# Optimization experiments

Hardware: AMD Instinct MI355X
Metric: run time of the kernel (lower is better)

## Reference

```python
import jax, jax.numpy as jnp
import numpy as np

B, S, HID = 2, 1024, 2048
N_HEADS, N_KV, HEAD_DIM = 32, 4, 128
BLOCK, MAX_BLOCKS = 32, 128
EPS = 1e-6
ROPE_THETA = 1e6


def _rmsnorm(x, w):
    # per-head RMSNorm over head_dim (Qwen3MoeRMSNorm)
    var = jnp.mean(x * x, axis=-1, keepdims=True)
    return x * jax.lax.rsqrt(var + EPS) * w


def _rotate_half(x):
    h = x.shape[-1] // 2
    return jnp.concatenate([-x[..., h:], x[..., :h]], axis=-1)


def setup_inputs() -> dict:
    key = jax.random.key(0)
    ks = jax.random.split(key, 8)
    hidden_states = jax.random.normal(ks[0], (B, S, HID), dtype=jnp.float32)
    wq = jax.random.normal(ks[1], (N_HEADS * HEAD_DIM, HID), dtype=jnp.float32) * 0.02
    wk = jax.random.normal(ks[2], (N_KV * HEAD_DIM, HID), dtype=jnp.float32) * 0.02
    wv = jax.random.normal(ks[3], (N_KV * HEAD_DIM, HID), dtype=jnp.float32) * 0.02
    wo = jax.random.normal(ks[4], (HID, N_HEADS * HEAD_DIM), dtype=jnp.float32) * 0.02
    q_norm_w = 1.0 + 0.01 * jax.random.normal(ks[5], (HEAD_DIM,), dtype=jnp.float32)
    k_norm_w = 1.0 + 0.01 * jax.random.normal(ks[6], (HEAD_DIM,), dtype=jnp.float32)
    # RoPE tables (rotate-half / llama convention)
    inv_freq = 1.0 / (ROPE_THETA ** (jnp.arange(0, HEAD_DIM, 2, dtype=jnp.float32) / HEAD_DIM))
    t = jnp.arange(S, dtype=jnp.float32)
    freqs = jnp.outer(t, inv_freq)  # [S, HEAD_DIM/2]
    emb = jnp.concatenate([freqs, freqs], axis=-1)  # [S, HEAD_DIM]
    cos, sin = jnp.cos(emb), jnp.sin(emb)
    # page table: B sequences x (S/BLOCK) blocks, distinct block ids
    page_table = jnp.arange(B * (S // BLOCK), dtype=jnp.int32).reshape(B, S // BLOCK)
    return {"hidden_states": hidden_states, "wq": wq, "wk": wk, "wv": wv, "wo": wo,
            "q_norm_w": q_norm_w, "k_norm_w": k_norm_w, "cos": cos, "sin": sin,
            "page_table": page_table}


def reference(hidden_states, wq, wk, wv, wo, q_norm_w, k_norm_w, cos, sin, page_table):
    b, s, _ = hidden_states.shape
    # fused QKV projection (math-equivalent to the concatenated qkv_proj_weight)
    q = (hidden_states @ wq.T).reshape(b, s, N_HEADS, HEAD_DIM)
    k = (hidden_states @ wk.T).reshape(b, s, N_KV, HEAD_DIM)
    v = (hidden_states @ wv.T).reshape(b, s, N_KV, HEAD_DIM)
    # per-head RMSNorm then RoPE
    q = _rmsnorm(q, q_norm_w)
    k = _rmsnorm(k, k_norm_w)
    c = cos[None, :, None, :]
    sn = sin[None, :, None, :]
    q = q * c + _rotate_half(q) * sn
    k = k * c + _rotate_half(k) * sn
    # paged KV-cache fill: [B, nblk, BLOCK, kvh, hd] -> cache[block_id, kvh, BLOCK, hd]
    nblk = s // BLOCK
    k_blk = k.reshape(b, nblk, BLOCK, N_KV, HEAD_DIM).transpose(0, 1, 3, 2, 4).reshape(-1, N_KV, BLOCK, HEAD_DIM)
    v_blk = v.reshape(b, nblk, BLOCK, N_KV, HEAD_DIM).transpose(0, 1, 3, 2, 4).reshape(-1, N_KV, BLOCK, HEAD_DIM)
    flat_pt = page_table.reshape(-1)
    cache_k = jnp.zeros((MAX_BLOCKS, N_KV, BLOCK, HEAD_DIM), dtype=k.dtype).at[flat_pt].set(k_blk)
    cache_v = jnp.zeros((MAX_BLOCKS, N_KV, BLOCK, HEAD_DIM), dtype=v.dtype).at[flat_pt].set(v_blk)
    # GQA: repeat kv heads (num_key_value_groups = 8)
    groups = N_HEADS // N_KV
    k_rep = jnp.repeat(k, groups, axis=2)  # [b, s, N_HEADS, hd]
    v_rep = jnp.repeat(v, groups, axis=2)
    # causal SDPA, scaling = head_dim ** -0.5
    scale = HEAD_DIM ** -0.5
    scores = jnp.einsum('bqhd,bkhd->bhqk', q, k_rep) * scale
    causal = jnp.tril(jnp.ones((s, s), dtype=bool))
    scores = jnp.where(causal[None, None], scores, jnp.finfo(scores.dtype).min)
    probs = jax.nn.softmax(scores, axis=-1)
    attn = jnp.einsum('bhqk,bkhd->bqhd', probs, v_rep).reshape(b, s, N_HEADS * HEAD_DIM)
    out = attn @ wo.T  # [b, s, HID]
    return out, cache_k, cache_v
```

## Files before the change

kernel.cpp:

```cpp
#include <hip/hip_runtime.h>
#include <hip/hip_bf16.h>


typedef __attribute__((ext_vector_type(8))) __bf16 bf16x8;
typedef __attribute__((ext_vector_type(4))) __bf16 bf16x4;
typedef __attribute__((ext_vector_type(4))) float f32x4;

__device__ __forceinline__ void gload16(const void* g, void* l) {
    __builtin_amdgcn_global_load_lds((const __attribute__((address_space(1))) void*)g,
                                     (__attribute__((address_space(3))) void*)l, 16, 0, 0);
}

__global__ __launch_bounds__(256) void cvt5(const float* __restrict__ s0, const float* __restrict__ s1,
                                            const float* __restrict__ s2, const float* __restrict__ s3,
                                            const float* __restrict__ s4,
                                            __bf16* __restrict__ d0, __bf16* __restrict__ d1,
                                            __bf16* __restrict__ d2, __bf16* __restrict__ d3,
                                            __bf16* __restrict__ d4) {
    const int b = blockIdx.x;
    const float* src; __bf16* dst; int off;
    if (b < 4096)       { src = s0; dst = d0; off = b; }
    else if (b < 12288) { src = s1; dst = d1; off = b - 4096; }
    else if (b < 13312) { src = s2; dst = d2; off = b - 12288; }
    else if (b < 14336) { src = s3; dst = d3; off = b - 13312; }
    else                { src = s4; dst = d4; off = b - 14336; }
    const int i = off * 256 + threadIdx.x;
    float4 v = reinterpret_cast<const float4*>(src)[i];
    bf16x4 o = {(__bf16)v.x, (__bf16)v.y, (__bf16)v.z, (__bf16)v.w};
    reinterpret_cast<bf16x4*>(dst)[i] = o;
}

__global__ __launch_bounds__(256) void reduce_add(float* __restrict__ o,
                                                  const float* __restrict__ p, int n4) {
    int i = blockIdx.x * 256 + threadIdx.x;
    int stride = gridDim.x * 256;
    for (; i < n4; i += stride) {
        float4 a = reinterpret_cast<float4*>(o)[i];
        float4 b = reinterpret_cast<const float4*>(p)[i];
        a.x += b.x; a.y += b.y; a.z += b.z; a.w += b.w;
        reinterpret_cast<float4*>(o)[i] = a;
    }
}

__global__ __launch_bounds__(512, 2) void gemm256(const __bf16* __restrict__ A,
                                                  const __bf16* __restrict__ B,
                                                  __bf16* __restrict__ C,
                                                  const int M, const int N, const int K) {
    __shared__ __bf16 Asm[2 * 256 * 64];
    __shared__ __bf16 Bsm[2 * 256 * 64];
    const int tid = threadIdx.x, lane = tid & 63, wave = tid >> 6;
    const int wm = wave >> 2, wn = wave & 3;
    const int lrow = lane & 15, lkg = lane >> 4;
    const int nbn = N >> 8;
    const int swz = ((int)blockIdx.x & 7) * ((int)gridDim.x >> 3) + ((int)blockIdx.x >> 3);
    const int bm = swz / nbn, bn = swz % nbn;
    const int brow = bm * 256, bcol = bn * 256;
    const int row0 = tid >> 3;
    const int scol_sw = ((tid & 7) ^ (row0 & 7)) * 8;
    const __bf16* gA = A + (size_t)(brow + row0) * K + scol_sw;
    const __bf16* gB = B + (size_t)(bcol + row0) * K + scol_sw;
    const int aslot0 = (lkg ^ (lrow & 7)) * 8;
    const int aslot1 = ((4 + lkg) ^ (lrow & 7)) * 8;
    const int nt = K / 64, nIter = nt / 2;

    f32x4 acc[8][4] = {};
    bf16x8 a[4][2];

    auto stage = [&](int s) {
        if (s >= 4 * nt) return;
        const int tau = s >> 2, h = s & 3, hb = s & 1;
        const size_t rofs = (size_t)(hb * 128) * K + (size_t)tau * 64;
        if (h < 2) {
            const __bf16* g = gA + rofs;
            __bf16* l = Asm + (tau & 1) * 16384 + hb * 8192 + tid * 8;
            gload16(g, l);
            gload16(g + (size_t)64 * K, l + 4096);
        } else {
            const __bf16* g = gB + rofs;
            __bf16* l = Bsm + (tau & 1) * 16384 + hb * 8192 + tid * 8;
            gload16(g, l);
            gload16(g + (size_t)64 * K, l + 4096);
        }
    };

    stage(0); stage(1); stage(2); stage(3); stage(4);
    asm volatile("s_waitcnt vmcnt(2)" ::: "memory");
    __builtin_amdgcn_s_barrier();

    for (int i = 0; i < nIter; ++i) {
        const bool last = (i == nIter - 1);
#pragma unroll
        for (int p = 0; p < 8; ++p) {
            const int q = p & 3, cbuf = p >> 2;
            const __bf16* As = Asm + cbuf * 16384;
            const __bf16* Bs = Bsm + cbuf * 16384;
            bf16x8 b[2][2];
            if ((q & 1) == 0) {
#pragma unroll
                for (int mf = 0; mf < 4; ++mf) {
                    const int r = wm * 128 + (q >> 1) * 64 + mf * 16 + lrow;
                    a[mf][0] = *reinterpret_cast<const bf16x8*>(&As[r * 64 + aslot0]);
                    a[mf][1] = *reinterpret_cast<const bf16x8*>(&As[r * 64 + aslot1]);
                }
            }
#pragma unroll
            for (int nf = 0; nf < 2; ++nf) {
                const int r = wn * 64 + (q & 1) * 32 + nf * 16 + lrow;
                b[nf][0] = *reinterpret_cast<const bf16x8*>(&Bs[r * 64 + aslot0]);
                b[nf][1] = *reinterpret_cast<const bf16x8*>(&Bs[r * 64 + aslot1]);
            }
            stage(8 * i + p + 5);
            if (p == 3) {
                if (last) asm volatile("s_waitcnt vmcnt(0)" ::: "memory");
                else      asm volatile("s_waitcnt vmcnt(2)" ::: "memory");
            } else if (p == 7 && !last) {
                asm volatile("s_waitcnt vmcnt(2)" ::: "memory");
            }
            __builtin_amdgcn_s_barrier();
            asm volatile("s_waitcnt lgkmcnt(0)" ::: "memory");
            __builtin_amdgcn_sched_barrier(0);
            __builtin_amdgcn_s_setprio(1);
#pragma unroll
            for (int mf = 0; mf < 4; ++mf)
#pragma unroll
                for (int nf = 0; nf < 2; ++nf)
#pragma unroll
                    for (int kk = 0; kk < 2; ++kk)
                        acc[(q >> 1) * 4 + mf][(q & 1) * 2 + nf] =
                            __builtin_amdgcn_mfma_f32_16x16x32_bf16(
                                a[mf][kk], b[nf][kk],
                                acc[(q >> 1) * 4 + mf][(q & 1) * 2 + nf], 0, 0, 0);
            __builtin_amdgcn_s_setprio(0);
            __builtin_amdgcn_s_barrier();
        }
    }
#pragma unroll
    for (int Mi = 0; Mi < 8; ++Mi)
#pragma unroll
        for (int Ni = 0; Ni < 4; ++Ni)
#pragma unroll
            for (int j = 0; j < 4; ++j) {
                const size_t r = brow + wm * 128 + Mi * 16 + lkg * 4 + j;
                const size_t c = bcol + wn * 64 + Ni * 16 + lrow;
                C[r * N + c] = (__bf16)acc[Mi][Ni][j];
            }
}

template <int OUT_BF16>
__global__ __launch_bounds__(256) void gemm_bt(const __bf16* __restrict__ A,
                                               const __bf16* __restrict__ B,
                                               void* __restrict__ C0,
                                               void* __restrict__ C1,
                                               const int M, const int N, const int K,
                                               const int klen) {
    __shared__ __bf16 As0[128 * 64];
    __shared__ __bf16 Bs0[128 * 64];
    __shared__ __bf16 As1[128 * 64];
    __shared__ __bf16 Bs1[128 * 64];
    const int tid = threadIdx.x;
    const int lane = tid & 63;
    const int wave = tid >> 6;
    const int bn = blockIdx.x, bm = blockIdx.y;
    const int kbeg = blockIdx.z * klen;
    const int brow = bm * 128, bcol = bn * 128;
    const int wr = wave >> 1, wc = wave & 1;
    const int lrow = lane & 15, lkg = lane >> 4;
    const int srow_in = lane >> 3;
    const int scol = (lane & 7) * 8;
    f32x4 acc[4][4] = {};

    auto stage = [&](int k0, __bf16* as, __bf16* bs) {
#pragma unroll
        for (int r = 0; r < 4; ++r) {
            const int chunk = r * 4 + wave;
            const int row = chunk * 8 + srow_in;
            gload16(&A[(size_t)(brow + row) * K + k0 + scol], as + chunk * 512);
            gload16(&B[(size_t)(bcol + row) * K + k0 + scol], bs + chunk * 512);
        }
    };
    auto compute = [&](const __bf16* as, const __bf16* bs) {
#pragma unroll
        for (int kk = 0; kk < 2; ++kk) {
            bf16x8 a[4], bfr[4];
#pragma unroll
            for (int m = 0; m < 4; ++m)
                a[m] = *reinterpret_cast<const bf16x8*>(&as[(wr * 64 + m * 16 + lrow) * 64 + kk * 32 + lkg * 8]);
#pragma unroll
            for (int n = 0; n < 4; ++n)
                bfr[n] = *reinterpret_cast<const bf16x8*>(&bs[(wc * 64 + n * 16 + lrow) * 64 + kk * 32 + lkg * 8]);
#pragma unroll
            for (int m = 0; m < 4; ++m)
#pragma unroll
                for (int n = 0; n < 4; ++n)
                    acc[m][n] = __builtin_amdgcn_mfma_f32_16x16x32_bf16(a[m], bfr[n], acc[m][n], 0, 0, 0);
        }
    };

    const int nt = klen / 64;
    stage(kbeg, As0, Bs0);
    asm volatile("s_waitcnt vmcnt(0)" ::: "memory");
    __syncthreads();
    int t = 0;
    for (; t + 2 < nt; t += 2) {
        stage(kbeg + (t + 1) * 64, As1, Bs1);
        compute(As0, Bs0);
        asm volatile("s_waitcnt vmcnt(0)" ::: "memory");
        __syncthreads();
        stage(kbeg + (t + 2) * 64, As0, Bs0);
        compute(As1, Bs1);
        asm volatile("s_waitcnt vmcnt(0)" ::: "memory");
        __syncthreads();
    }
    stage(kbeg + (t + 1) * 64, As1, Bs1);
    compute(As0, Bs0);
    asm volatile("s_waitcnt vmcnt(0)" ::: "memory");
    __syncthreads();
    compute(As1, Bs1);

    void* C = blockIdx.z == 0 ? C0 : C1;
#pragma unroll
    for (int m = 0; m < 4; ++m)
#pragma unroll
        for (int n = 0; n < 4; ++n)
#pragma unroll
            for (int j = 0; j < 4; ++j) {
                const size_t r = brow + wr * 64 + m * 16 + lkg * 4 + j;
                const size_t c = bcol + wc * 64 + n * 16 + lrow;
                if (OUT_BF16)
                    ((__bf16*)C)[r * N + c] = (__bf16)acc[m][n][j];
                else
                    ((float*)C)[r * N + c] = acc[m][n][j];
            }
}

__global__ __launch_bounds__(256) void norm_rope_cache(
    __bf16* __restrict__ qkv, const float* __restrict__ cosT, const float* __restrict__ sinT,
    const float* __restrict__ qw, const float* __restrict__ kw,
    const int* __restrict__ ptab, float* __restrict__ cacheK, float* __restrict__ cacheV) {
    const int t = blockIdx.x;
    const int b = t >> 10, s = t & 1023;
    const int wave = threadIdx.x >> 6, lane = threadIdx.x & 63;
    __bf16* row = qkv + (size_t)t * 5120;
    const float c = cosT[s * 128 + lane];
    const float sn = sinT[s * 128 + lane];
    const int page = ptab[b * 32 + (s >> 5)];
    const int so = s & 31;
    const float wq0 = qw[lane], wq1 = qw[lane + 64];
#pragma unroll
    for (int i = 0; i < 8; ++i) {
        const int h = wave * 8 + i;
        float x0 = (float)row[h * 128 + lane];
        float x1 = (float)row[h * 128 + 64 + lane];
        float ss = x0 * x0 + x1 * x1;
        for (int off = 32; off; off >>= 1) ss += __shfl_xor(ss, off);
        const float rs = rsqrtf(ss * (1.0f / 128.0f) + 1e-6f);
        const float y0 = x0 * rs * wq0, y1 = x1 * rs * wq1;
        row[h * 128 + lane]      = (__bf16)(y0 * c - y1 * sn);
        row[h * 128 + 64 + lane] = (__bf16)(y1 * c + y0 * sn);
    }
    {
        const int h = wave;
        float x0 = (float)row[4096 + h * 128 + lane];
        float x1 = (float)row[4096 + h * 128 + 64 + lane];
        float ss = x0 * x0 + x1 * x1;
        for (int off = 32; off; off >>= 1) ss += __shfl_xor(ss, off);
        const float rs = rsqrtf(ss * (1.0f / 128.0f) + 1e-6f);
        const float y0 = x0 * rs * kw[lane], y1 = x1 * rs * kw[lane + 64];
        const float o0 = y0 * c - y1 * sn, o1 = y1 * c + y0 * sn;
        row[4096 + h * 128 + lane]      = (__bf16)o0;
        row[4096 + h * 128 + 64 + lane] = (__bf16)o1;
        float* ck = cacheK + (((size_t)page * 4 + h) * 32 + so) * 128;
        ck[lane] = o0; ck[lane + 64] = o1;
        const float v0 = (float)row[4608 + h * 128 + lane];
        const float v1 = (float)row[4608 + h * 128 + 64 + lane];
        float* cv = cacheV + (((size_t)page * 4 + h) * 32 + so) * 128;
        cv[lane] = v0; cv[lane + 64] = v1;
    }
}

__global__ __launch_bounds__(512, 2) void attn_fwd(const __bf16* __restrict__ qkv,
                                                   __bf16* __restrict__ out) {
    __shared__ __bf16 Ks[2][64 * 128];
    __shared__ __bf16 Vs[2][128 * 64];
    __shared__ __bf16 Ps[8][2][16 * 64];
    const int qa = blockIdx.x;
    const int qbig = 63 - qa;
    const int kvg = blockIdx.y, b = blockIdx.z;
    const int tid = threadIdx.x, wave = tid >> 6, lane = tid & 63;
    const int lrow = lane & 15, lkg = lane >> 4;
    const int h = kvg * 8 + wave;
    const size_t base = (size_t)b * 1024 * 5120;
    const int kofs = 4096 + kvg * 128, vofs = 4608 + kvg * 128;
    const int ntA = qa / 4 + 1, nt = qbig / 4 + 1;
    const int qposA = qa * 16 + lrow, qposB = qbig * 16 + lrow;
    const int rsw = lrow & 7;

    bf16x8 aqA[4], aqB[4];
#pragma unroll
    for (int kc = 0; kc < 4; ++kc) {
        bf16x8 ta = *reinterpret_cast<const bf16x8*>(
            &qkv[base + (size_t)(qa * 16 + lrow) * 5120 + h * 128 + kc * 32 + lkg * 8]);
        bf16x8 tb = *reinterpret_cast<const bf16x8*>(
            &qkv[base + (size_t)(qbig * 16 + lrow) * 5120 + h * 128 + kc * 32 + lkg * 8]);
#pragma unroll
        for (int i = 0; i < 8; ++i) {
            ta[i] = (__bf16)((float)ta[i] * 0.08838834764831845f);
            tb[i] = (__bf16)((float)tb[i] * 0.08838834764831845f);
        }
        aqA[kc] = ta; aqB[kc] = tb;
    }

    f32x4 accA[8] = {}, accB[8] = {};
    float mA = -1e30f, lA = 0.f, mB = -1e30f, lB = 0.f;
    __bf16* PwA = &Ps[wave][0][0];
    __bf16* PwB = &Ps[wave][1][0];

    auto stageK = [&](int t, int buf) {
        const int kv0 = (t < nt) ? t * 64 : 0;
#pragma unroll
        for (int c = 0; c < 2; ++c) {
            const int chunk = c * 8 + wave;
            const int row = chunk * 4 + (lane >> 4);
            const int gslot = (lane & 15) ^ (row & 7);
            gload16(&qkv[base + (size_t)(kv0 + row) * 5120 + kofs + gslot * 8],
                    &Ks[buf][chunk * 512]);
        }
    };
    auto loadV = [&](int t, uint4 (&vr)[2]) {
        const int kv0 = (t < nt) ? t * 64 : 0;
#pragma unroll
        for (int r = 0; r < 2; ++r)
            vr[r] = *reinterpret_cast<const uint4*>(
                &qkv[base + (size_t)(kv0 + lane) * 5120 + vofs + wave * 16 + r * 8]);
    };
    auto writeV = [&](uint4 (&vr)[2], int buf) {
#pragma unroll
        for (int r = 0; r < 2; ++r) {
            const __bf16* pv = reinterpret_cast<const __bf16*>(&vr[r]);
#pragma unroll
            for (int j = 0; j < 8; ++j) {
                const int d = wave * 16 + r * 8 + j;
                Vs[buf][d * 64 + (((lane >> 3) ^ j) << 3) + (lane & 7)] = pv[j];
            }
        }
    };

    auto smax = [&](f32x4 (&st)[4], float& m_i, float& l_i, f32x4 (&acc)[8],
                    int qpos, int kv0, bool maskit, __bf16* Pw) {
        float sv[16]; float pmax = -1e30f;
#pragma unroll
        for (int f = 0; f < 4; ++f)
#pragma unroll
            for (int j = 0; j < 4; ++j) {
                float x = st[f][j];
                if (maskit) {
                    const int kvpos = kv0 + f * 16 + lkg * 4 + j;
                    if (kvpos > qpos) x = -1e30f;
                }
                sv[f * 4 + j] = x;
                pmax = fmaxf(pmax, x);
            }
        pmax = fmaxf(pmax, __shfl_xor(pmax, 16));
        pmax = fmaxf(pmax, __shfl_xor(pmax, 32));
        if (!__all(pmax - m_i <= 8.f)) {
            const float m_new = fmaxf(m_i, pmax);
            const float sf = __expf(m_i - m_new);
            m_i = m_new;
            l_i *= sf;
            float sfj[4];
#pragma unroll
            for (int j = 0; j < 4; ++j) sfj[j] = __shfl(sf, lkg * 4 + j);
#pragma unroll
            for (int f = 0; f < 8; ++f)
#pragma unroll
                for (int j = 0; j < 4; ++j) acc[f][j] *= sfj[j];
        }
        float ladd = 0.f;
#pragma unroll
        for (int f = 0; f < 4; ++f) {
            bf16x4 pb;
#pragma unroll
            for (int j = 0; j < 4; ++j) {
                const float p = __expf(sv[f * 4 + j] - m_i);
                ladd += p;
                pb[j] = (__bf16)p;
            }
            const int slot = (f * 2 + (lkg >> 1)) ^ rsw;
            *reinterpret_cast<bf16x4*>(&Pw[lrow * 64 + slot * 8 + (lkg & 1) * 4]) = pb;
        }
        ladd += __shfl_xor(ladd, 16);
        ladd += __shfl_xor(ladd, 32);
        l_i += ladd;
    };

    auto body = [&](int t, uint4 (&vcur)[2], uint4 (&vnext)[2]) {
        const int kbuf = t & 1;
        __builtin_amdgcn_s_barrier();
        asm volatile("" ::: "memory");
        loadV(t + 1, vnext);
        stageK(t + 1, kbuf ^ 1);
        asm volatile("s_waitcnt vmcnt(4)" ::: "memory");
        writeV(vcur, kbuf);
        asm volatile("s_waitcnt lgkmcnt(0)" ::: "memory");
        __builtin_amdgcn_s_barrier();
        asm volatile("" ::: "memory");

        const bool doA = t < ntA;
        f32x4 stA[4] = {}, stB[4] = {};
#pragma unroll
        for (int kc = 0; kc < 4; ++kc)
#pragma unroll
            for (int f = 0; f < 4; ++f) {
                bf16x8 ak = *reinterpret_cast<const bf16x8*>(
                    &Ks[kbuf][(f * 16 + lrow) * 128 + (((kc * 4 + lkg) ^ rsw) << 3)]);
                stB[f] = __builtin_amdgcn_mfma_f32_16x16x32_bf16(ak, aqB[kc], stB[f], 0, 0, 0);
                if (doA)
                    stA[f] = __builtin_amdgcn_mfma_f32_16x16x32_bf16(ak, aqA[kc], stA[f], 0, 0, 0);
            }
        if (doA) smax(stA, mA, lA, accA, qposA, t * 64, t == ntA - 1, PwA);
        smax(stB, mB, lB, accB, qposB, t * 64, t == nt - 1, PwB);
#pragma unroll
        for (int kk = 0; kk < 2; ++kk) {
            const int pslot = ((kk * 4 + lkg) ^ rsw) << 3;
            bf16x8 apB = *reinterpret_cast<const bf16x8*>(&PwB[lrow * 64 + pslot]);
            bf16x8 apA;
            if (doA) apA = *reinterpret_cast<const bf16x8*>(&PwA[lrow * 64 + pslot]);
#pragma unroll
            for (int f = 0; f < 8; ++f) {
                bf16x8 bv = *reinterpret_cast<const bf16x8*>(
                    &Vs[kbuf][(f * 16 + lrow) * 64 + pslot]);
                accB[f] = __builtin_amdgcn_mfma_f32_16x16x32_bf16(apB, bv, accB[f], 0, 0, 0);
                if (doA)
                    accA[f] = __builtin_amdgcn_mfma_f32_16x16x32_bf16(apA, bv, accA[f], 0, 0, 0);
            }
        }
    };

    uint4 vrA[2], vrB[2];
    loadV(0, vrA);
    stageK(0, 0);
    for (int t = 0; t < nt; t += 2) {
        body(t, vrA, vrB);
        if (t + 1 < nt) body(t + 1, vrB, vrA);
    }
    asm volatile("s_waitcnt vmcnt(0)" ::: "memory");

    float linvA[4], linvB[4];
#pragma unroll
    for (int j = 0; j < 4; ++j) {
        linvA[j] = 1.0f / __shfl(lA, lkg * 4 + j);
        linvB[j] = 1.0f / __shfl(lB, lkg * 4 + j);
    }
#pragma unroll
    for (int f = 0; f < 8; ++f)
#pragma unroll
        for (int j = 0; j < 4; ++j) {
            out[((size_t)b * 1024 + qa * 16 + lkg * 4 + j) * 4096 + h * 128 + f * 16 + lrow] =
                (__bf16)(accA[f][j] * linvA[j]);
            out[((size_t)b * 1024 + qbig * 16 + lkg * 4 + j) * 4096 + h * 128 + f * 16 + lrow] =
                (__bf16)(accB[f][j] * linvB[j]);
        }
}

extern "C" void kernel_launch(void* const* d_in, const int* in_sizes, int n_in,
                              void* d_out, int out_size, void* d_ws, size_t ws_size,
                              hipStream_t stream) {
    const float* hidden = (const float*)d_in[0];
    const float* wq = (const float*)d_in[1];
    const float* wk = (const float*)d_in[2];
    const float* wv = (const float*)d_in[3];
    const float* wo = (const float*)d_in[4];
    const float* qnw = (const float*)d_in[5];
    const float* knw = (const float*)d_in[6];
    const float* cosT = (const float*)d_in[7];
    const float* sinT = (const float*)d_in[8];
    const int* ptab = (const int*)d_in[9];

    float* outp = (float*)d_out;
    float* cacheK = outp + 4194304;
    float* cacheV = cacheK + 2097152;

    char* ws = (char*)d_ws;
    __bf16* hbf    = (__bf16*)ws;
    __bf16* w1bf   = (__bf16*)(ws + 8388608);
    __bf16* wobf   = (__bf16*)(ws + 29360128);
    __bf16* qkvbf  = (__bf16*)(ws + 46137344);
    __bf16* attnbf = (__bf16*)ws;
    float*  opart  = (float*)(ws + 46137344);

    cvt5<<<22528, 256, 0, stream>>>(hidden, wq, wk, wv, wo,
                                    hbf, w1bf, w1bf + (size_t)4096 * 2048,
                                    w1bf + (size_t)4608 * 2048, wobf);

    gemm256<<<160, 512, 0, stream>>>(hbf, w1bf, qkvbf, 2048, 5120, 2048);

    hipMemsetAsync(cacheK, 0, (size_t)4194304 * 4, stream);
    norm_rope_cache<<<2048, 256, 0, stream>>>(qkvbf, cosT, sinT, qnw, knw, ptab, cacheK, cacheV);

    attn_fwd<<<dim3(32, 4, 2), 512, 0, stream>>>(qkvbf, attnbf);

    gemm_bt<0><<<dim3(16, 16, 2), 256, 0, stream>>>(attnbf, wobf, outp, opart,
                                                    2048, 2048, 4096, 2048);
    reduce_add<<<2048, 256, 0, stream>>>(outp, opart, 4194304 / 4);
}
```

Measured before the change: 206.6 us.

## Unify GEMMs into templated 8-wave pipelined kernel with smaller tiles

Replaces the 256x256 QKV GEMM and the 128x128 output-projection GEMM with one templated 512-thread kernel. It uses a 128-row tile and an NF*64-column tile (320 for QKV, 256 for the output projection), with a finer-grained staged global-to-LDS load schedule and split-K support. The QKV grid grows from 160 to 256 blocks, which should fill the CUs better. The output projection gets the deeper pipelined 8-wave schedule in place of the simple double-buffered kernel. In exchange, each tile has lower arithmetic intensity and the load issue pattern is more intricate.

```diff
diff --git a/kernel.cpp b/kernel.cpp
--- a/kernel.cpp
+++ b/kernel.cpp
@@ -42,48 +42,52 @@
     }
 }
 
-__global__ __launch_bounds__(512, 2) void gemm256(const __bf16* __restrict__ A,
-                                                  const __bf16* __restrict__ B,
-                                                  __bf16* __restrict__ C,
-                                                  const int M, const int N, const int K) {
-    __shared__ __bf16 Asm[2 * 256 * 64];
-    __shared__ __bf16 Bsm[2 * 256 * 64];
+template <int NF, int OUT_BF16>
+__global__ __launch_bounds__(512, 2) void gemm8p(const __bf16* __restrict__ A,
+                                                 const __bf16* __restrict__ B,
+                                                 void* __restrict__ C0,
+                                                 void* __restrict__ C1,
+                                                 const int M, const int N, const int K,
+                                                 const int nTiles, const int nbn,
+                                                 const int klen) {
+    __shared__ __bf16 Asm[2 * 128 * 64];
+    __shared__ __bf16 Bsm[2 * NF * 64 * 64];
     const int tid = threadIdx.x, lane = tid & 63, wave = tid >> 6;
     const int wm = wave >> 2, wn = wave & 3;
     const int lrow = lane & 15, lkg = lane >> 4;
-    const int nbn = N >> 8;
-    const int swz = ((int)blockIdx.x & 7) * ((int)gridDim.x >> 3) + ((int)blockIdx.x >> 3);
-    const int bm = swz / nbn, bn = swz % nbn;
-    const int brow = bm * 256, bcol = bn * 256;
+    const int rsw = lrow & 7;
+    const int bid = blockIdx.x;
+    const int kz = bid / nTiles, tile = bid % nTiles;
+    const int tswz = (tile & 7) * (nTiles >> 3) + (tile >> 3);
+    const int bm = tswz / nbn, bn = tswz % nbn;
+    const int brow = bm * 128, bcol = bn * (NF * 64);
+    const int kbeg = kz * klen;
     const int row0 = tid >> 3;
     const int scol_sw = ((tid & 7) ^ (row0 & 7)) * 8;
-    const __bf16* gA = A + (size_t)(brow + row0) * K + scol_sw;
-    const __bf16* gB = B + (size_t)(bcol + row0) * K + scol_sw;
-    const int aslot0 = (lkg ^ (lrow & 7)) * 8;
-    const int aslot1 = ((4 + lkg) ^ (lrow & 7)) * 8;
-    const int nt = K / 64, nIter = nt / 2;
-
-    f32x4 acc[8][4] = {};
-    bf16x8 a[4][2];
-
-    auto stage = [&](int s) {
-        if (s >= 4 * nt) return;
-        const int tau = s >> 2, h = s & 3, hb = s & 1;
-        const size_t rofs = (size_t)(hb * 128) * K + (size_t)tau * 64;
-        if (h < 2) {
-            const __bf16* g = gA + rofs;
-            __bf16* l = Asm + (tau & 1) * 16384 + hb * 8192 + tid * 8;
-            gload16(g, l);
-            gload16(g + (size_t)64 * K, l + 4096);
-        } else {
-            const __bf16* g = gB + rofs;
-            __bf16* l = Bsm + (tau & 1) * 16384 + hb * 8192 + tid * 8;
-            gload16(g, l);
-            gload16(g + (size_t)64 * K, l + 4096);
-        }
-    };
-
-    stage(0); stage(1); stage(2); stage(3); stage(4);
+    const __bf16* gA = A + (size_t)(brow + row0) * K + kbeg + scol_sw;
+    const __bf16* gB = B + (size_t)(bcol + row0) * K + kbeg + scol_sw;
+    const int slot0 = (lkg ^ rsw) * 8;
+    const int slot1 = ((4 + lkg) ^ rsw) * 8;
+    const int nt = klen / 64, nIter = nt / 2;
+
+    f32x4 acc[4][NF] = {};
+    bf16x8 areg[2], breg[NF];
+
+    int su_t = 0, su_w = 0;
+    auto stage1 = [&]() {
+        if (su_t < nt) {
+            const size_t ko = (size_t)su_t * 64;
+            if (su_w < 2)
+                gload16(gA + (size_t)(su_w * 64) * K + ko,
+                        Asm + (su_t & 1) * 8192 + su_w * 4096 + tid * 8);
+            else
+                gload16(gB + (size_t)((su_w - 2) * 64) * K + ko,
+                        Bsm + (su_t & 1) * (NF * 4096) + (su_w - 2) * 4096 + tid * 8);
+        }
+        if (++su_w == NF + 2) { su_w = 0; ++su_t; }
+    };
+
+    for (int u = 0; u < NF + 4; ++u) stage1();
     asm volatile("s_waitcnt vmcnt(2)" ::: "memory");
     __builtin_amdgcn_s_barrier();
 
@@ -91,25 +95,24 @@
         const bool last = (i == nIter - 1);
 #pragma unroll
         for (int p = 0; p < 8; ++p) {
-            const int q = p & 3, cbuf = p >> 2;
-            const __bf16* As = Asm + cbuf * 16384;
-            const __bf16* Bs = Bsm + cbuf * 16384;
-            bf16x8 b[2][2];
-            if ((q & 1) == 0) {
-#pragma unroll
-                for (int mf = 0; mf < 4; ++mf) {
-                    const int r = wm * 128 + (q >> 1) * 64 + mf * 16 + lrow;
-                    a[mf][0] = *reinterpret_cast<const bf16x8*>(&As[r * 64 + aslot0]);
-                    a[mf][1] = *reinterpret_cast<const bf16x8*>(&As[r * 64 + aslot1]);
-                }
-            }
-#pragma unroll
-            for (int nf = 0; nf < 2; ++nf) {
-                const int r = wn * 64 + (q & 1) * 32 + nf * 16 + lrow;
-                b[nf][0] = *reinterpret_cast<const bf16x8*>(&Bs[r * 64 + aslot0]);
-                b[nf][1] = *reinterpret_cast<const bf16x8*>(&Bs[r * 64 + aslot1]);
-            }
-            stage(8 * i + p + 5);
+            const int q = p & 3, kk = q >> 1, mfh = q & 1, cbuf = p >> 2;
+            const __bf16* As = Asm + cbuf * 8192;
+            const __bf16* Bs = Bsm + cbuf * (NF * 4096);
+            const int ks = kk ? slot1 : slot0;
+            if (mfh == 0) {
+#pragma unroll
+                for (int nf = 0; nf < NF; ++nf)
+                    breg[nf] = *reinterpret_cast<const bf16x8*>(
+                        &Bs[(wn * (NF * 16) + nf * 16 + lrow) * 64 + ks]);
+            }
+#pragma unroll
+            for (int mi = 0; mi < 2; ++mi)
+                areg[mi] = *reinterpret_cast<const bf16x8*>(
+                    &As[(wm * 64 + (mfh * 2 + mi) * 16 + lrow) * 64 + ks]);
+            const int cp = (NF == 5) ? ((q == 2) ? 1 : 2)
+                                     : ((q == 1 || q == 2) ? 1 : 2);
+            stage1();
+            if (cp == 2) stage1();
             if (p == 3) {
                 if (last) asm volatile("s_waitcnt vmcnt(0)" ::: "memory");
                 else      asm volatile("s_waitcnt vmcnt(2)" ::: "memory");
@@ -121,115 +124,29 @@
             __builtin_amdgcn_sched_barrier(0);
             __builtin_amdgcn_s_setprio(1);
 #pragma unroll
-            for (int mf = 0; mf < 4; ++mf)
-#pragma unroll
-                for (int nf = 0; nf < 2; ++nf)
-#pragma unroll
-                    for (int kk = 0; kk < 2; ++kk)
-                        acc[(q >> 1) * 4 + mf][(q & 1) * 2 + nf] =
-                            __builtin_amdgcn_mfma_f32_16x16x32_bf16(
-                                a[mf][kk], b[nf][kk],
-                                acc[(q >> 1) * 4 + mf][(q & 1) * 2 + nf], 0, 0, 0);
+            for (int mi = 0; mi < 2; ++mi)
+#pragma unroll
+                for (int nf = 0; nf < NF; ++nf)
+                    acc[mfh * 2 + mi][nf] = __builtin_amdgcn_mfma_f32_16x16x32_bf16(
+                        areg[mi], breg[nf], acc[mfh * 2 + mi][nf], 0, 0, 0);
             __builtin_amdgcn_s_setprio(0);
             __builtin_amdgcn_s_barrier();
         }
     }
-#pragma unroll
-    for (int Mi = 0; Mi < 8; ++Mi)
-#pragma unroll
-        for (int Ni = 0; Ni < 4; ++Ni)
+
+    void* C = (kz == 0) ? C0 : C1;
+#pragma unroll
+    for (int mi = 0; mi < 4; ++mi)
+#pragma unroll
+        for (int nf = 0; nf < NF; ++nf)
 #pragma unroll
             for (int j = 0; j < 4; ++j) {
-                const size_t r = brow + wm * 128 + Mi * 16 + lkg * 4 + j;
-                const size_t c = bcol + wn * 64 + Ni * 16 + lrow;
-                C[r * N + c] = (__bf16)acc[Mi][Ni][j];
-            }
-}
-
-template <int OUT_BF16>
-__global__ __launch_bounds__(256) void gemm_bt(const __bf16* __restrict__ A,
-                                               const __bf16* __restrict__ B,
-                                               void* __restrict__ C0,
-                                               void* __restrict__ C1,
-                                               const int M, const int N, const int K,
-                                               const int klen) {
-    __shared__ __bf16 As0[128 * 64];
-    __shared__ __bf16 Bs0[128 * 64];
-    __shared__ __bf16 As1[128 * 64];
-    __shared__ __bf16 Bs1[128 * 64];
-    const int tid = threadIdx.x;
-    const int lane = tid & 63;
-    const int wave = tid >> 6;
-    const int bn = blockIdx.x, bm = blockIdx.y;
-    const int kbeg = blockIdx.z * klen;
-    const int brow = bm * 128, bcol = bn * 128;
-    const int wr = wave >> 1, wc = wave & 1;
-    const int lrow = lane & 15, lkg = lane >> 4;
-    const int srow_in = lane >> 3;
-    const int scol = (lane & 7) * 8;
-    f32x4 acc[4][4] = {};
-
-    auto stage = [&](int k0, __bf16* as, __bf16* bs) {
-#pragma unroll
-        for (int r = 0; r < 4; ++r) {
-            const int chunk = r * 4 + wave;
-            const int row = chunk * 8 + srow_in;
-            gload16(&A[(size_t)(brow + row) * K + k0 + scol], as + chunk * 512);
-            gload16(&B[(size_t)(bcol + row) * K + k0 + scol], bs + chunk * 512);
-        }
-    };
-    auto compute = [&](const __bf16* as, const __bf16* bs) {
-#pragma unroll
-        for (int kk = 0; kk < 2; ++kk) {
-            bf16x8 a[4], bfr[4];
-#pragma unroll
-            for (int m = 0; m < 4; ++m)
-                a[m] = *reinterpret_cast<const bf16x8*>(&as[(wr * 64 + m * 16 + lrow) * 64 + kk * 32 + lkg * 8]);
-#pragma unroll
-            for (int n = 0; n < 4; ++n)
-                bfr[n] = *reinterpret_cast<const bf16x8*>(&bs[(wc * 64 + n * 16 + lrow) * 64 + kk * 32 + lkg * 8]);
-#pragma unroll
-            for (int m = 0; m < 4; ++m)
-#pragma unroll
-                for (int n = 0; n < 4; ++n)
-                    acc[m][n] = __builtin_amdgcn_mfma_f32_16x16x32_bf16(a[m], bfr[n], acc[m][n], 0, 0, 0);
-        }
-    };
-
-    const int nt = klen / 64;
-    stage(kbeg, As0, Bs0);
-    asm volatile("s_waitcnt vmcnt(0)" ::: "memory");
-    __syncthreads();
-    int t = 0;
-    for (; t + 2 < nt; t += 2) {
-        stage(kbeg + (t + 1) * 64, As1, Bs1);
-        compute(As0, Bs0);
-        asm volatile("s_waitcnt vmcnt(0)" ::: "memory");
-        __syncthreads();
-        stage(kbeg + (t + 2) * 64, As0, Bs0);
-        compute(As1, Bs1);
-        asm volatile("s_waitcnt vmcnt(0)" ::: "memory");
-        __syncthreads();
-    }
-    stage(kbeg + (t + 1) * 64, As1, Bs1);
-    compute(As0, Bs0);
-    asm volatile("s_waitcnt vmcnt(0)" ::: "memory");
-    __syncthreads();
-    compute(As1, Bs1);
-
-    void* C = blockIdx.z == 0 ? C0 : C1;
-#pragma unroll
-    for (int m = 0; m < 4; ++m)
-#pragma unroll
-        for (int n = 0; n < 4; ++n)
-#pragma unroll
-            for (int j = 0; j < 4; ++j) {
-                const size_t r = brow + wr * 64 + m * 16 + lkg * 4 + j;
-                const size_t c = bcol + wc * 64 + n * 16 + lrow;
+                const size_t r = brow + wm * 64 + mi * 16 + lkg * 4 + j;
+                const size_t c = bcol + wn * (NF * 16) + nf * 16 + lrow;
                 if (OUT_BF16)
-                    ((__bf16*)C)[r * N + c] = (__bf16)acc[m][n][j];
+                    ((__bf16*)C)[r * N + c] = (__bf16)acc[mi][nf][j];
                 else
-                    ((float*)C)[r * N + c] = acc[m][n][j];
+                    ((float*)C)[r * N + c] = acc[mi][nf][j];
             }
 }
 
@@ -492,14 +409,15 @@
                                     hbf, w1bf, w1bf + (size_t)4096 * 2048,
                                     w1bf + (size_t)4608 * 2048, wobf);
 
-    gemm256<<<160, 512, 0, stream>>>(hbf, w1bf, qkvbf, 2048, 5120, 2048);
+    gemm8p<5, 1><<<256, 512, 0, stream>>>(hbf, w1bf, qkvbf, nullptr,
+                                          2048, 5120, 2048, 256, 16, 2048);
 
     hipMemsetAsync(cacheK, 0, (size_t)4194304 * 4, stream);
     norm_rope_cache<<<2048, 256, 0, stream>>>(qkvbf, cosT, sinT, qnw, knw, ptab, cacheK, cacheV);
 
     attn_fwd<<<dim3(32, 4, 2), 512, 0, stream>>>(qkvbf, attnbf);
 
-    gemm_bt<0><<<dim3(16, 16, 2), 256, 0, stream>>>(attnbf, wobf, outp, opart,
-                                                    2048, 2048, 4096, 2048);
+    gemm8p<4, 0><<<256, 512, 0, stream>>>(attnbf, wobf, outp, opart,
+                                          2048, 2048, 4096, 128, 8, 2048);
     reduce_add<<<2048, 256, 0, stream>>>(outp, opart, 4194304 / 4);
 }
```

After: 201.7 us. 1.02x faster.
